# Optimization experiments

Hardware: AMD Instinct MI355X
Metric: run time of the kernel (lower is better)

Reference implementation:

```python
import jax, jax.numpy as jnp
import numpy as np

N_USERS, N_NEWS, N_ENT, N_REL, D, K, NNZ = 10000, 10000, 100000, 32, 64, 20, 500000

def setup_inputs() -> dict:
    key = jax.random.key(0)
    ks = jax.random.split(key, 10)
    return {
        "user_emb": jax.random.normal(ks[0], (N_USERS, D), jnp.float32),
        "news_embeding": jax.random.normal(ks[1], (N_NEWS, D), jnp.float32),
        "entity_emb": jax.random.normal(ks[2], (N_ENT, D), jnp.float32),
        "relation_emb": jax.random.normal(ks[3], (N_REL, D), jnp.float32),
        "news_entities": jax.random.randint(ks[4], (N_NEWS, K), 0, N_ENT),
        "news_relations": jnp.zeros((N_NEWS, K), jnp.int32),  # code forces relation id 0 for news
        "neigh_entities": jax.random.randint(ks[5], (N_ENT, K), 0, N_ENT),
        "neigh_relations": jax.random.randint(ks[6], (N_ENT, K), 0, N_REL),
        "interact_rows": jax.random.randint(ks[7], (NNZ,), 0, N_USERS),
        "interact_cols": jax.random.randint(ks[8], (NNZ,), 0, N_NEWS),
        "interact_vals": jax.random.uniform(ks[9], (NNZ,), jnp.float32),
    }

def _sim_hrt(head, tail, rel):
    # head: [N,D], tail/rel: [N,K,D]
    tail_rel = tail * rel                              # [N,K,D]
    head_rel = head[:, None, :] * rel                  # [N,K,D]
    # NOTE: original norms over the NEIGHBOR dim (dim=1), yielding [N,1,D]
    hnorm = jnp.sqrt(jnp.sum(head_rel * head_rel, axis=1))  # [N,D]
    att = jnp.einsum('nkd,nd->nk', tail_rel, hnorm)    # [N,K]
    return att * att

def _agg(head_emb, neigh_ent_emb, neigh_rel_emb):
    w = jax.nn.softmax(_sim_hrt(head_emb, neigh_ent_emb, neigh_rel_emb), axis=-1)
    return jnp.einsum('nk,nkd->nd', w, neigh_ent_emb)

def reference(user_emb, news_embeding, entity_emb, relation_emb,
              news_entities, news_relations, neigh_entities, neigh_relations,
              interact_rows, interact_cols, interact_vals):
    # news aggregation (newsid = arange -> identity gather on news_embeding)
    news_ne = entity_emb[news_entities]                # [N_news,K,D]
    news_nr = relation_emb[news_relations]             # [N_news,K,D]
    news_agg = _agg(news_embeding, news_ne, news_nr)   # [N_news,D]
    # entity aggregation (entities = arange -> identity gather on entity_emb)
    ent_ne = entity_emb[neigh_entities]                # [N_ent,K,D]
    ent_nr = relation_emb[neigh_relations]             # [N_ent,K,D]
    entity_agg = _agg(entity_emb, ent_ne, ent_nr)      # [N_ent,D]
    # user aggregation: sparse interact_mat @ news_agg via segment_sum
    gathered = interact_vals[:, None] * news_agg[interact_cols]  # [NNZ,D]
    user_agg = jax.ops.segment_sum(gathered, interact_rows, num_segments=N_USERS)
    score = jax.nn.softmax(user_emb @ news_agg.T, axis=-1)       # [N_users,N_news]
    user_agg = user_agg + (score @ news_agg) * user_agg
    return (news_agg, entity_agg, user_agg)
```

## Files before the change

### kernel.cpp

```cpp
#include <hip/hip_runtime.h>
#include <hip/hip_bf16.h>


#define DD 64
#define KK 20
#define NCHUNK 313
#define NSL 20
#define NSTRIP 157
#define NUPAD 10048
#define ATSTRIDE 10016
#define PST32 20

typedef __attribute__((ext_vector_type(8))) short short8;
typedef __attribute__((ext_vector_type(4))) float f32x4;

__device__ __forceinline__ unsigned short f2bf(float x) {
    union { __hip_bfloat16 h; unsigned short u; } cv;
    cv.h = __float2bfloat16(x);
    return cv.u;
}
__device__ __forceinline__ float bfu2f(unsigned short u) {
    return __uint_as_float(((unsigned)u) << 16);
}
#define MFMA16(a, b, c) __builtin_amdgcn_mfma_f32_16x16x32_bf16((a), (b), (c), 0, 0, 0)

__global__ __launch_bounds__(256)
void agg_kernel(const float* __restrict__ head_emb, const float* __restrict__ ent_emb,
                const float* __restrict__ rel_emb,
                const int* __restrict__ ent_idx, const int* __restrict__ rel_idx,
                float* __restrict__ outp, int N)
{
    int w = threadIdx.x >> 6;
    int lane = threadIdx.x & 63;
    int half = lane >> 5;
    int l = lane & 31;
    int n0 = blockIdx.x * 8 + w * 2;
    if (n0 >= N) return;

    float2 head = *(const float2*)(head_emb + (long)(n0 + half) * DD + 2 * l);

    float2 tail[KK], trp[KK];
    float2 s2 = make_float2(0.f, 0.f);
#pragma unroll
    for (int k = 0; k < KK; ++k) {
        int ei0 = ent_idx[n0 * KK + k];
        int ei1 = ent_idx[(n0 + 1) * KK + k];
        int ri0 = rel_idx[n0 * KK + k];
        int ri1 = rel_idx[(n0 + 1) * KK + k];
        int e = half ? ei1 : ei0;
        int r = half ? ri1 : ri0;
        float2 rv = *(const float2*)(rel_emb + (long)r * DD + 2 * l);
        float2 tv = *(const float2*)(ent_emb + (long)e * DD + 2 * l);
        tail[k] = tv;
        trp[k] = make_float2(tv.x * rv.x, tv.y * rv.y);
        s2.x = fmaf(rv.x, rv.x, s2.x);
        s2.y = fmaf(rv.y, rv.y, s2.y);
    }
    float2 hn;
    hn.x = fabsf(head.x) * sqrtf(s2.x);
    hn.y = fabsf(head.y) * sqrtf(s2.y);

    float att[KK];
#pragma unroll
    for (int k = 0; k < KK; ++k) {
        float v = fmaf(trp[k].y, hn.y, trp[k].x * hn.x);
#pragma unroll
        for (int m = 1; m < 32; m <<= 1)
            v += __shfl_xor(v, m, 64);
        att[k] = v * v;
    }
    float mx = att[0];
#pragma unroll
    for (int k = 1; k < KK; ++k) mx = fmaxf(mx, att[k]);
    float den = 0.f;
#pragma unroll
    for (int k = 0; k < KK; ++k) { att[k] = __expf(att[k] - mx); den += att[k]; }
    float inv = 1.f / den;
    float2 o = make_float2(0.f, 0.f);
#pragma unroll
    for (int k = 0; k < KK; ++k) {
        o.x = fmaf(att[k], tail[k].x, o.x);
        o.y = fmaf(att[k], tail[k].y, o.y);
    }
    o.x *= inv; o.y *= inv;
    *(float2*)(outp + (long)(n0 + half) * DD + 2 * l) = o;
}

__global__ __launch_bounds__(256)
void cvt_kernel(const float* __restrict__ src, unsigned short* __restrict__ dst,
                int n_src, int n_total)
{
    int t = blockIdx.x * 256 + threadIdx.x;
    if (t >= n_total) return;
    float v = (t < n_src) ? src[t] : 0.f;
    dst[t] = f2bf(v);
}

__global__ __launch_bounds__(256)
void transpose_kernel(const float* __restrict__ src, unsigned short* __restrict__ AT)
{
    __shared__ float T[128][65];
    int t = threadIdx.x;
    int nb = blockIdx.x * 128;
    const float4* s4 = (const float4*)src;
#pragma unroll
    for (int i = 0; i < 8; ++i) {
        int f = i * 256 + t;
        int row = f >> 4;
        int c4 = f & 15;
        int gr = nb + row;
        float4 v = make_float4(0.f, 0.f, 0.f, 0.f);
        if (gr < 10000) v = s4[(long)gr * 16 + c4];
        T[row][c4 * 4 + 0] = v.x;
        T[row][c4 * 4 + 1] = v.y;
        T[row][c4 * 4 + 2] = v.z;
        T[row][c4 * 4 + 3] = v.w;
    }
    __syncthreads();
    int d = t >> 2;
    int seg = t & 3;
#pragma unroll
    for (int g = 0; g < 8; ++g) {
        int nl = seg * 32 + g * 4;
        int n = nb + nl;
        if (n + 3 < ATSTRIDE) {
            int base = seg * 32;
            ushort4 oh;
            oh.x = f2bf(T[base + 2 * g][d]);
            oh.y = f2bf(T[base + 16 + 2 * g][d]);
            oh.z = f2bf(T[base + 2 * g + 1][d]);
            oh.w = f2bf(T[base + 16 + 2 * g + 1][d]);
            *(ushort4*)(AT + (long)d * ATSTRIDE + n) = oh;
        }
    }
}

__global__ __launch_bounds__(256)
void hist_kernel(const int* __restrict__ rows, int* __restrict__ cnt, int nnz)
{
    int e = blockIdx.x * 256 + threadIdx.x;
    if (e < nnz) atomicAdd(&cnt[rows[e]], 1);
}

__global__ __launch_bounds__(256)
void scan_kernel(const int* __restrict__ cnt, int* __restrict__ offs, int* __restrict__ cur)
{
    __shared__ int ssum[256];
    int t = threadIdx.x;
    int loc[40];
    int s = 0;
#pragma unroll
    for (int i = 0; i < 40; ++i) { loc[i] = s; s += cnt[t * 40 + i]; }
    ssum[t] = s;
    __syncthreads();
    int val = s;
    for (int off = 1; off < 256; off <<= 1) {
        int v = (t >= off) ? ssum[t - off] : 0;
        __syncthreads();
        val += v;
        ssum[t] = val;
        __syncthreads();
    }
    int excl = val - s;
#pragma unroll
    for (int i = 0; i < 40; ++i) {
        int o = excl + loc[i];
        offs[t * 40 + i] = o;
        cur[t * 40 + i] = o;
    }
}

__global__ __launch_bounds__(256)
void fill_kernel(const int* __restrict__ rows, int* __restrict__ cur,
                 int* __restrict__ eid, int nnz)
{
    int e = blockIdx.x * 256 + threadIdx.x;
    if (e < nnz) {
        int p = atomicAdd(&cur[rows[e]], 1);
        eid[p] = e;
    }
}

__global__ __launch_bounds__(256)
void gather_kernel(const int* __restrict__ offs, const int* __restrict__ eid,
                   const int* __restrict__ cols, const float* __restrict__ vals,
                   const float* __restrict__ A, float* __restrict__ seg, int n_users)
{
    int w = threadIdx.x >> 6;
    int lane = threadIdx.x & 63;
    int u = blockIdx.x * 4 + w;
    if (u >= n_users) return;
    int s0 = offs[u], s1 = offs[u + 1];
    float acc = 0.f;
    for (int i = s0; i < s1; ++i) {
        int e = eid[i];
        float v = vals[e];
        int c = cols[e];
        acc = fmaf(v, A[(long)c * DD + lane], acc);
    }
    seg[(long)u * DD + lane] = acc;
}

__global__ __launch_bounds__(256)
void attn_kernel(const unsigned short* __restrict__ Ubf,
                 const unsigned short* __restrict__ Bbf,
                 const unsigned short* __restrict__ ATbf,
                 float* __restrict__ num, float* __restrict__ den)
{
    __shared__ __align__(16) unsigned int Pu[4][2][16 * PST32];

    int w = threadIdx.x >> 6;
    int lane = threadIdx.x & 63;
    int quad = lane >> 4;
    int l15 = lane & 15;
    int wid = blockIdx.x * 4 + w;
    if (wid >= NSTRIP * NSL) return;
    int strip = wid % NSTRIP;
    int slice = wid / NSTRIP;
    int user0 = strip * 64;

    short8 ua0[4], ua1[4];
#pragma unroll
    for (int t = 0; t < 4; ++t) {
        const short* up = (const short*)Ubf + ((long)(user0 + t * 16 + l15)) * 64;
        ua0[t] = *(const short8*)(up + quad * 8);
        ua1[t] = *(const short8*)(up + 32 + quad * 8);
    }

    f32x4 numC[4][4];
    float dena[4][4];
#pragma unroll
    for (int t = 0; t < 4; ++t)
#pragma unroll
        for (int c = 0; c < 4; ++c) {
            numC[t][c] = (f32x4){0.f, 0.f, 0.f, 0.f};
            dena[t][c] = 0.f;
        }

    for (int ch = slice; ch < NCHUNK; ch += NSL) {
        int nb = ch * 32;
        const short* bh = (const short*)Bbf + ((long)(nb + l15)) * 64;
        short8 b00 = *(const short8*)(bh + quad * 8);
        short8 b01 = *(const short8*)(bh + 32 + quad * 8);
        short8 b10 = *(const short8*)(bh + 16 * 64 + quad * 8);
        short8 b11 = *(const short8*)(bh + 16 * 64 + 32 + quad * 8);

        short8 vh[4];
#pragma unroll
        for (int c = 0; c < 4; ++c)
            vh[c] = *(const short8*)((const short*)ATbf +
                    ((long)(16 * c + l15)) * ATSTRIDE + nb + quad * 8);

        bool vlo = (nb + l15) < 10000;
        bool vhi = (nb + 16 + l15) < 10000;
        f32x4 z = {0.f, 0.f, 0.f, 0.f};
#pragma unroll
        for (int p = 0; p < 2; ++p) {
#pragma unroll
            for (int tt = 0; tt < 2; ++tt) {
                int t = p * 2 + tt;
                f32x4 Llo = MFMA16(ua0[t], b00, z);
                Llo = MFMA16(ua1[t], b01, Llo);
                f32x4 Lhi = MFMA16(ua0[t], b10, z);
                Lhi = MFMA16(ua1[t], b11, Lhi);
                unsigned int* Pt = Pu[w][tt];
#pragma unroll
                for (int r = 0; r < 4; ++r) {
                    float plo = vlo ? __expf(fminf(Llo[r], 70.f)) : 0.f;
                    float phi = vhi ? __expf(fminf(Lhi[r], 70.f)) : 0.f;
                    __hip_bfloat162 pk2 = __float22bfloat162_rn(make_float2(plo, phi));
                    unsigned int pk;
                    __builtin_memcpy(&pk, &pk2, 4);
                    Pt[(quad * 4 + r) * PST32 + l15] = pk;
                    dena[t][r] += __uint_as_float(pk << 16)
                                + __uint_as_float(pk & 0xffff0000u);
                }
            }
            short8 ap[2];
#pragma unroll
            for (int tt = 0; tt < 2; ++tt)
                ap[tt] = *(const short8*)((const short*)Pu[w][tt] +
                         l15 * (PST32 * 2) + quad * 8);
#pragma unroll
            for (int c = 0; c < 4; ++c)
#pragma unroll
                for (int tt = 0; tt < 2; ++tt)
                    numC[p * 2 + tt][c] = MFMA16(ap[tt], vh[c], numC[p * 2 + tt][c]);
        }
    }

#pragma unroll
    for (int t = 0; t < 4; ++t)
#pragma unroll
        for (int r = 0; r < 4; ++r) {
#pragma unroll
            for (int m = 1; m < 16; m <<= 1)
                dena[t][r] += __shfl_xor(dena[t][r], m, 64);
        }
    if (l15 == 0) {
#pragma unroll
        for (int t = 0; t < 4; ++t)
#pragma unroll
            for (int r = 0; r < 4; ++r)
                atomicAdd(&den[user0 + t * 16 + quad * 4 + r], dena[t][r]);
    }
#pragma unroll
    for (int t = 0; t < 4; ++t)
#pragma unroll
        for (int c = 0; c < 4; ++c)
#pragma unroll
            for (int r = 0; r < 4; ++r)
                atomicAdd(&num[(long)(user0 + t * 16 + quad * 4 + r) * DD + c * 16 + l15],
                          numC[t][c][r]);
}

__global__ __launch_bounds__(256)
void final_kernel(const float* __restrict__ seg, const float* __restrict__ num,
                  const float* __restrict__ den, float* __restrict__ out, int n_users)
{
    int t = blockIdx.x * 256 + threadIdx.x;
    if (t >= n_users * DD) return;
    int u = t >> 6;
    float s = seg[t];
    float o2 = num[t] / den[u];
    out[t] = fmaf(s, o2, s);
}

extern "C" void kernel_launch(void* const* d_in, const int* in_sizes, int n_in,
                              void* d_out, int out_size, void* d_ws, size_t ws_size,
                              hipStream_t stream)
{
    const float* user_emb = (const float*)d_in[0];
    const float* news_emb = (const float*)d_in[1];
    const float* ent_emb  = (const float*)d_in[2];
    const float* rel_emb  = (const float*)d_in[3];
    const int* news_entities   = (const int*)d_in[4];
    const int* news_relations  = (const int*)d_in[5];
    const int* neigh_entities  = (const int*)d_in[6];
    const int* neigh_relations = (const int*)d_in[7];
    const int* interact_rows   = (const int*)d_in[8];
    const int* interact_cols   = (const int*)d_in[9];
    const float* interact_vals = (const float*)d_in[10];

    const int NU = 10000, NN = 10000, NE = 100000, NNZ = 500000;

    float* out_news = (float*)d_out;
    float* out_ent  = out_news + (long)NN * DD;
    float* out_user = out_ent + (long)NE * DD;

    float* seg  = out_ent;
    float* num  = seg + 640000;
    float* den  = num + 643072;
    int*   cnt  = (int*)(den + 10240);
    int*   offs = cnt + 10240;
    int*   cur  = offs + 10240;
    int*   eid  = cur + 10240;
    unsigned short* Ubf  = (unsigned short*)(eid + 500000);
    unsigned short* Bbf  = Ubf + 643072;
    unsigned short* ATbf = Bbf + 641024;

    hipMemsetAsync(num, 0, (size_t)(643072 + 10240 + 10240) * sizeof(float), stream);

    agg_kernel<<<NN / 8, 256, 0, stream>>>(news_emb, ent_emb, rel_emb,
                                           news_entities, news_relations, out_news, NN);
    cvt_kernel<<<(NUPAD * DD + 255) / 256, 256, 0, stream>>>(user_emb, Ubf, NU * DD, NUPAD * DD);
    cvt_kernel<<<2504, 256, 0, stream>>>(out_news, Bbf, NN * DD, 10016 * DD);
    transpose_kernel<<<(NN + 127) / 128, 256, 0, stream>>>(out_news, ATbf);
    hist_kernel<<<(NNZ + 255) / 256, 256, 0, stream>>>(interact_rows, cnt, NNZ);
    scan_kernel<<<1, 256, 0, stream>>>(cnt, offs, cur);
    fill_kernel<<<(NNZ + 255) / 256, 256, 0, stream>>>(interact_rows, cur, eid, NNZ);
    gather_kernel<<<(NU + 3) / 4, 256, 0, stream>>>(offs, eid, interact_cols,
                                                    interact_vals, out_news, seg, NU);
    attn_kernel<<<(NSTRIP * NSL + 3) / 4, 256, 0, stream>>>(Ubf, Bbf, ATbf, num, den);
    final_kernel<<<(NU * DD + 255) / 256, 256, 0, stream>>>(seg, num, den, out_user, NU);
    agg_kernel<<<NE / 8, 256, 0, stream>>>(ent_emb, ent_emb, rel_emb,
                                           neigh_entities, neigh_relations, out_ent, NE);
}
```

Baseline: 464.5 us.

## Fuse news bf16 conversion into transpose, enlarge blocks, use workspace scratch

The separate cvt_kernel pass that converts news_agg to row-major bf16 is removed, and the transpose kernel now writes that copy from its shared-memory tile, which saves one launch and one read of news_agg. Most elementwise, atomic and aggregation kernels move from 256-thread to 1024-thread blocks to reduce block count. Scratch buffers move to the provided workspace when it is large enough, instead of aliasing the entity output. The larger blocks can lower occupancy and scheduling flexibility for the register-heavy agg_kernel.

```diff
diff --git a/kernel.cpp b/kernel.cpp
--- a/kernel.cpp
+++ b/kernel.cpp
@@ -10,6 +10,7 @@
 #define NUPAD 10048
 #define ATSTRIDE 10016
 #define PST32 20
+#define ATTN_BLOCKS 785
 
 typedef __attribute__((ext_vector_type(8))) short short8;
 typedef __attribute__((ext_vector_type(4))) float f32x4;
@@ -24,7 +25,7 @@
 }
 #define MFMA16(a, b, c) __builtin_amdgcn_mfma_f32_16x16x32_bf16((a), (b), (c), 0, 0, 0)
 
-__global__ __launch_bounds__(256)
+__global__ __launch_bounds__(1024)
 void agg_kernel(const float* __restrict__ head_emb, const float* __restrict__ ent_emb,
                 const float* __restrict__ rel_emb,
                 const int* __restrict__ ent_idx, const int* __restrict__ rel_idx,
@@ -34,7 +35,7 @@
     int lane = threadIdx.x & 63;
     int half = lane >> 5;
     int l = lane & 31;
-    int n0 = blockIdx.x * 8 + w * 2;
+    int n0 = blockIdx.x * 32 + w * 2;
     if (n0 >= N) return;
 
     float2 head = *(const float2*)(head_emb + (long)(n0 + half) * DD + 2 * l);
@@ -86,18 +87,19 @@
     *(float2*)(outp + (long)(n0 + half) * DD + 2 * l) = o;
 }
 
-__global__ __launch_bounds__(256)
+__global__ __launch_bounds__(1024)
 void cvt_kernel(const float* __restrict__ src, unsigned short* __restrict__ dst,
                 int n_src, int n_total)
 {
-    int t = blockIdx.x * 256 + threadIdx.x;
+    int t = blockIdx.x * 1024 + threadIdx.x;
     if (t >= n_total) return;
     float v = (t < n_src) ? src[t] : 0.f;
     dst[t] = f2bf(v);
 }
 
 __global__ __launch_bounds__(256)
-void transpose_kernel(const float* __restrict__ src, unsigned short* __restrict__ AT)
+void transpose_kernel(const float* __restrict__ src, unsigned short* __restrict__ Bbf,
+                      unsigned short* __restrict__ AT)
 {
     __shared__ float T[128][65];
     int t = threadIdx.x;
@@ -117,6 +119,21 @@
         T[row][c4 * 4 + 3] = v.w;
     }
     __syncthreads();
+#pragma unroll
+    for (int i = 0; i < 8; ++i) {
+        int f = i * 256 + t;
+        int row = f >> 4;
+        int q4 = f & 15;
+        int gr = nb + row;
+        if (gr < 10016) {
+            ushort4 ob;
+            ob.x = f2bf(T[row][q4 * 4 + 0]);
+            ob.y = f2bf(T[row][q4 * 4 + 1]);
+            ob.z = f2bf(T[row][q4 * 4 + 2]);
+            ob.w = f2bf(T[row][q4 * 4 + 3]);
+            *(ushort4*)(Bbf + (long)gr * 64 + q4 * 4) = ob;
+        }
+    }
     int d = t >> 2;
     int seg = t & 3;
 #pragma unroll
@@ -135,10 +152,10 @@
     }
 }
 
-__global__ __launch_bounds__(256)
+__global__ __launch_bounds__(1024)
 void hist_kernel(const int* __restrict__ rows, int* __restrict__ cnt, int nnz)
 {
-    int e = blockIdx.x * 256 + threadIdx.x;
+    int e = blockIdx.x * 1024 + threadIdx.x;
     if (e < nnz) atomicAdd(&cnt[rows[e]], 1);
 }
 
@@ -170,25 +187,25 @@
     }
 }
 
-__global__ __launch_bounds__(256)
+__global__ __launch_bounds__(1024)
 void fill_kernel(const int* __restrict__ rows, int* __restrict__ cur,
                  int* __restrict__ eid, int nnz)
 {
-    int e = blockIdx.x * 256 + threadIdx.x;
+    int e = blockIdx.x * 1024 + threadIdx.x;
     if (e < nnz) {
         int p = atomicAdd(&cur[rows[e]], 1);
         eid[p] = e;
     }
 }
 
-__global__ __launch_bounds__(256)
+__global__ __launch_bounds__(1024)
 void gather_kernel(const int* __restrict__ offs, const int* __restrict__ eid,
                    const int* __restrict__ cols, const float* __restrict__ vals,
                    const float* __restrict__ A, float* __restrict__ seg, int n_users)
 {
     int w = threadIdx.x >> 6;
     int lane = threadIdx.x & 63;
-    int u = blockIdx.x * 4 + w;
+    int u = blockIdx.x * 16 + w;
     if (u >= n_users) return;
     int s0 = offs[u], s1 = offs[u + 1];
     float acc = 0.f;
@@ -314,11 +331,11 @@
                           numC[t][c][r]);
 }
 
-__global__ __launch_bounds__(256)
+__global__ __launch_bounds__(1024)
 void final_kernel(const float* __restrict__ seg, const float* __restrict__ num,
                   const float* __restrict__ den, float* __restrict__ out, int n_users)
 {
-    int t = blockIdx.x * 256 + threadIdx.x;
+    int t = blockIdx.x * 1024 + threadIdx.x;
     if (t >= n_users * DD) return;
     int u = t >> 6;
     float s = seg[t];
@@ -348,7 +365,15 @@
     float* out_ent  = out_news + (long)NN * DD;
     float* out_user = out_ent + (long)NE * DD;
 
-    float* seg  = out_ent;
+    const size_t SCRATCH_F32 =
+        640000 + 643072 + 10240 + 10240 + 10240 + 10240 + 500000;
+    const size_t SCRATCH_BYTES = SCRATCH_F32 * 4 +
+        (size_t)(643072 + 641024 + 641024) * 2;
+
+    bool use_ws = (d_ws != nullptr) && (ws_size >= SCRATCH_BYTES);
+    float* base = use_ws ? (float*)d_ws : out_ent;
+
+    float* seg  = base;
     float* num  = seg + 640000;
     float* den  = num + 643072;
     int*   cnt  = (int*)(den + 10240);
@@ -361,18 +386,20 @@
 
     hipMemsetAsync(num, 0, (size_t)(643072 + 10240 + 10240) * sizeof(float), stream);
 
-    agg_kernel<<<NN / 8, 256, 0, stream>>>(news_emb, ent_emb, rel_emb,
-                                           news_entities, news_relations, out_news, NN);
-    cvt_kernel<<<(NUPAD * DD + 255) / 256, 256, 0, stream>>>(user_emb, Ubf, NU * DD, NUPAD * DD);
-    cvt_kernel<<<2504, 256, 0, stream>>>(out_news, Bbf, NN * DD, 10016 * DD);
-    transpose_kernel<<<(NN + 127) / 128, 256, 0, stream>>>(out_news, ATbf);
-    hist_kernel<<<(NNZ + 255) / 256, 256, 0, stream>>>(interact_rows, cnt, NNZ);
+    agg_kernel<<<(NN + 31) / 32, 1024, 0, stream>>>(news_emb, ent_emb, rel_emb,
+                                                    news_entities, news_relations,
+                                                    out_news, NN);
+    cvt_kernel<<<(NUPAD * DD + 1023) / 1024, 1024, 0, stream>>>(user_emb, Ubf,
+                                                                NU * DD, NUPAD * DD);
+    transpose_kernel<<<(NN + 127) / 128, 256, 0, stream>>>(out_news, Bbf, ATbf);
+    hist_kernel<<<(NNZ + 1023) / 1024, 1024, 0, stream>>>(interact_rows, cnt, NNZ);
     scan_kernel<<<1, 256, 0, stream>>>(cnt, offs, cur);
-    fill_kernel<<<(NNZ + 255) / 256, 256, 0, stream>>>(interact_rows, cur, eid, NNZ);
-    gather_kernel<<<(NU + 3) / 4, 256, 0, stream>>>(offs, eid, interact_cols,
-                                                    interact_vals, out_news, seg, NU);
-    attn_kernel<<<(NSTRIP * NSL + 3) / 4, 256, 0, stream>>>(Ubf, Bbf, ATbf, num, den);
-    final_kernel<<<(NU * DD + 255) / 256, 256, 0, stream>>>(seg, num, den, out_user, NU);
-    agg_kernel<<<NE / 8, 256, 0, stream>>>(ent_emb, ent_emb, rel_emb,
-                                           neigh_entities, neigh_relations, out_ent, NE);
-}
+    fill_kernel<<<(NNZ + 1023) / 1024, 1024, 0, stream>>>(interact_rows, cur, eid, NNZ);
+    gather_kernel<<<(NU + 15) / 16, 1024, 0, stream>>>(offs, eid, interact_cols,
+                                                       interact_vals, out_news, seg, NU);
+    attn_kernel<<<ATTN_BLOCKS, 256, 0, stream>>>(Ubf, Bbf, ATbf, num, den);
+    final_kernel<<<(NU * DD + 1023) / 1024, 1024, 0, stream>>>(seg, num, den, out_user, NU);
+    agg_kernel<<<(NE + 31) / 32, 1024, 0, stream>>>(ent_emb, ent_emb, rel_emb,
+                                                    neigh_entities, neigh_relations,
+                                                    out_ent, NE);
+}
```

After: 513.8 us. 1.11x slower.
